# Optimization experiments

Measured on AMD Instinct MI355X. Metric: run time of the kernel, lower is better.

Reference implementation:

```python
import jax, jax.numpy as jnp
import numpy as np

HID, NH, HD = 1024, 16, 64
WIN = 512
DFF, NE, TOPK = 4096, 8, 2
B, S = 1, 2048
EPS = 1e-6


def _rope_rotation_matrix(seq_len, head_dim):
    # Block-diagonal 2x2 rotation matrices per position (standard RoPE as a fused matrix).
    pos = np.arange(seq_len, dtype=np.float64)
    inv_freq = 1.0 / (10000.0 ** (np.arange(0, head_dim, 2, dtype=np.float64) / head_dim))
    ang = pos[:, None] * inv_freq[None, :]            # [S, HD/2]
    c, s = np.cos(ang), np.sin(ang)
    R = np.zeros((seq_len, head_dim, head_dim), np.float32)
    i = np.arange(0, head_dim, 2)
    R[:, i, i] = c
    R[:, i + 1, i + 1] = c
    R[:, i, i + 1] = -s
    R[:, i + 1, i] = s
    return jnp.asarray(R)


def setup_inputs() -> dict:
    key = jax.random.key(0)
    ks = jax.random.split(key, 10)
    init = lambda k, shape, scale=0.02: (jax.random.normal(k, shape, jnp.float32) * scale)
    return {
        "x": jax.random.normal(ks[0], (B, S, HID), jnp.float32),
        "rotation_matrix": _rope_rotation_matrix(S, HD),
        "rms1_w": jnp.ones((HID,), jnp.float32),
        "wq": init(ks[1], (HID, HID)),
        "wk": init(ks[2], (HID, HID)),
        "wv": init(ks[3], (HID, HID)),
        "wo": init(ks[4], (HID, HID)),
        "rms2_w": jnp.ones((HID,), jnp.float32),
        "gate_w": init(ks[5], (HID, NE)),
        "w1": init(ks[6], (NE, HID, DFF)),
        "w2": init(ks[7], (NE, DFF, HID)),
        "w3": init(ks[8], (NE, HID, DFF)),
    }


def _rmsnorm(x, w):
    return x * jax.lax.rsqrt(jnp.mean(x * x, axis=-1, keepdims=True) + EPS) * w


def reference(x, rotation_matrix, rms1_w, wq, wk, wv, wo, rms2_w, gate_w, w1, w2, w3):
    b, s, _ = x.shape
    # --- sliding-window attention with fused RoPE rotation matrix ---
    y = _rmsnorm(x, rms1_w)
    q = (y @ wq).reshape(b, s, NH, HD).transpose(0, 2, 1, 3)  # bhsd
    k = (y @ wk).reshape(b, s, NH, HD).transpose(0, 2, 1, 3)
    v = (y @ wv).reshape(b, s, NH, HD).transpose(0, 2, 1, 3)
    q = jnp.einsum('bhsd,sde->bhse', q, rotation_matrix)
    k = jnp.einsum('bhsd,sde->bhse', k, rotation_matrix)
    scores = jnp.einsum('bhqd,bhkd->bhqk', q, k) / np.float32(np.sqrt(HD))
    idx = jnp.arange(s)
    mask = (idx[:, None] >= idx[None, :]) & (idx[:, None] - idx[None, :] < WIN)
    scores = jnp.where(mask[None, None], scores, jnp.float32(-1e9))
    att = jax.nn.softmax(scores, axis=-1)
    attn_out = jnp.einsum('bhqk,bhkd->bhqd', att, v)
    attn_out = attn_out.transpose(0, 2, 1, 3).reshape(b, s, HID) @ wo
    x = x + attn_out
    # --- MoE SwiGLU FFN with top-k routing ---
    y = _rmsnorm(x, rms2_w)
    t = y.reshape(b * s, HID)                                  # [T, D]
    logits = t @ gate_w                                        # [T, E]
    top_v, top_i = jax.lax.top_k(logits, TOPK)
    gates = jax.nn.softmax(top_v, axis=-1)                     # [T, K]
    w_full = jnp.zeros((b * s, NE), t.dtype).at[
        jnp.arange(b * s)[:, None], top_i].set(gates)          # [T, E] sparse routing weights
    h = jax.nn.silu(jnp.einsum('td,edf->etf', t, w1)) * jnp.einsum('td,edf->etf', t, w3)
    expert_out = jnp.einsum('etf,efd->etd', h, w2)             # [E, T, D]
    moe = jnp.einsum('te,etd->td', w_full, expert_out).reshape(b, s, HID)
    return x + moe
```

## Files before the change

kernel.cpp:

```cpp
#include <hip/hip_runtime.h>
#include <hip/hip_bf16.h>
#include <stdint.h>


#define S_ 2048
#define HID_ 1024
#define NH_ 16
#define HD_ 64
#define WIN_ 512
#define DFF_ 4096
#define NE_ 8

typedef unsigned short u16;
typedef __attribute__((ext_vector_type(8))) short short8;
typedef __attribute__((ext_vector_type(4))) float f32x4;

__device__ __forceinline__ u16 f2bf(float f) {
  union { float f; unsigned u; } v; v.f = f;
  unsigned r = (v.u + 0x7FFFu + ((v.u >> 16) & 1u)) >> 16;
  return (u16)r;
}
__device__ __forceinline__ float bf2f(u16 b) {
  union { unsigned u; float f; } v; v.u = ((unsigned)b) << 16;
  return v.f;
}

__device__ __forceinline__ void gload16(const void* g, void* l) {
  __builtin_amdgcn_global_load_lds(
      (const __attribute__((address_space(1))) void*)g,
      (__attribute__((address_space(3))) void*)l, 16, 0, 0);
}

__global__ __launch_bounds__(256) void convT_f32_k(const float* __restrict__ W,
                                                   u16* __restrict__ WT,
                                                   int K, int N, size_t matStride) {
  __shared__ u16 t[64][66];
  const float* Wm = W + (size_t)blockIdx.z * matStride;
  u16* WTm = WT + (size_t)blockIdx.z * matStride;
  int n0 = blockIdx.x * 64, k0 = blockIdx.y * 64;
  int tid = threadIdx.x;
  int c2 = (tid & 31) * 2, rr = tid >> 5;
#pragma unroll
  for (int it = 0; it < 8; ++it) {
    int r = it * 8 + rr;
    float2 ab = *(const float2*)&Wm[(size_t)(k0 + r) * N + n0 + c2];
    t[c2][r] = f2bf(ab.x);
    t[c2 + 1][r] = f2bf(ab.y);
  }
  __syncthreads();
#pragma unroll
  for (int it = 0; it < 8; ++it) {
    int n = it * 8 + rr;
    unsigned pk = (unsigned)t[n][c2] | ((unsigned)t[n][c2 + 1] << 16);
    *(unsigned*)&WTm[(size_t)(n0 + n) * K + k0 + c2] = pk;
  }
}

__global__ __launch_bounds__(256) void convT_u16_k(const u16* __restrict__ W,
                                                   u16* __restrict__ WT,
                                                   int K, int N, size_t matStride) {
  __shared__ u16 t[64][66];
  const u16* Wm = W + (size_t)blockIdx.z * matStride;
  u16* WTm = WT + (size_t)blockIdx.z * matStride;
  int n0 = blockIdx.x * 64, k0 = blockIdx.y * 64;
  int tid = threadIdx.x;
  int c2 = (tid & 31) * 2, rr = tid >> 5;
#pragma unroll
  for (int it = 0; it < 8; ++it) {
    int r = it * 8 + rr;
    unsigned vv = *(const unsigned*)&Wm[(size_t)(k0 + r) * N + n0 + c2];
    t[c2][r] = (u16)vv;
    t[c2 + 1][r] = (u16)(vv >> 16);
  }
  __syncthreads();
#pragma unroll
  for (int it = 0; it < 8; ++it) {
    int n = it * 8 + rr;
    unsigned pk = (unsigned)t[n][c2] | ((unsigned)t[n][c2 + 1] << 16);
    *(unsigned*)&WTm[(size_t)(n0 + n) * K + k0 + c2] = pk;
  }
}

__global__ __launch_bounds__(256) void rope_tab_k(const float* __restrict__ rot,
                                                  float* __restrict__ cost,
                                                  float* __restrict__ sint) {
  int id = blockIdx.x * 256 + threadIdx.x;
  if (id >= S_ * 32) return;
  int s = id >> 5, j = id & 31;
  cost[id] = rot[(size_t)s * 4096 + (size_t)(2 * j) * 64 + 2 * j];
  sint[id] = rot[(size_t)s * 4096 + (size_t)(2 * j + 1) * 64 + 2 * j];
}

__global__ __launch_bounds__(256) void rms1_k(const float* __restrict__ x,
                                              const float* __restrict__ rw,
                                              u16* __restrict__ y) {
  int row = blockIdx.x, tid = threadIdx.x;
  const float4 v = *(const float4*)&x[(size_t)row * HID_ + tid * 4];
  float ss = v.x * v.x + v.y * v.y + v.z * v.z + v.w * v.w;
#pragma unroll
  for (int o = 32; o; o >>= 1) ss += __shfl_xor(ss, o);
  __shared__ float red[4];
  if ((tid & 63) == 0) red[tid >> 6] = ss;
  __syncthreads();
  float rstd = rsqrtf((red[0] + red[1] + red[2] + red[3]) * (1.f / HID_) + 1e-6f);
  const float4 w4 = *(const float4*)&rw[tid * 4];
  ushort4 o4;
  o4.x = f2bf(v.x * rstd * w4.x);
  o4.y = f2bf(v.y * rstd * w4.y);
  o4.z = f2bf(v.z * rstd * w4.z);
  o4.w = f2bf(v.w * rstd * w4.w);
  *(ushort4*)&y[(size_t)row * HID_ + tid * 4] = o4;
}

__global__ __launch_bounds__(256) void rms2_gate_k(const float* __restrict__ x2,
                                                   const float* __restrict__ rw,
                                                   const float* __restrict__ gw,
                                                   u16* __restrict__ y2,
                                                   float* __restrict__ logits) {
  int row = blockIdx.x, tid = threadIdx.x;
  int wv = tid >> 6, ln = tid & 63;
  const float4 v = *(const float4*)&x2[(size_t)row * HID_ + tid * 4];
  float ss = v.x * v.x + v.y * v.y + v.z * v.z + v.w * v.w;
#pragma unroll
  for (int o = 32; o; o >>= 1) ss += __shfl_xor(ss, o);
  __shared__ float red[4];
  __shared__ float lred[4][8];
  if (ln == 0) red[wv] = ss;
  __syncthreads();
  float rstd = rsqrtf((red[0] + red[1] + red[2] + red[3]) * (1.f / HID_) + 1e-6f);
  const float4 w4 = *(const float4*)&rw[tid * 4];
  float yv[4];
  yv[0] = v.x * rstd * w4.x; yv[1] = v.y * rstd * w4.y;
  yv[2] = v.z * rstd * w4.z; yv[3] = v.w * rstd * w4.w;
  ushort4 o4;
  o4.x = f2bf(yv[0]); o4.y = f2bf(yv[1]); o4.z = f2bf(yv[2]); o4.w = f2bf(yv[3]);
  *(ushort4*)&y2[(size_t)row * HID_ + tid * 4] = o4;
  float le[8] = {0, 0, 0, 0, 0, 0, 0, 0};
  int d0 = tid * 4;
#pragma unroll
  for (int j = 0; j < 4; ++j) {
    const float* grow = &gw[(size_t)(d0 + j) * NE_];
#pragma unroll
    for (int e = 0; e < 8; ++e) le[e] += yv[j] * grow[e];
  }
#pragma unroll
  for (int e = 0; e < 8; ++e) {
    float t = le[e];
#pragma unroll
    for (int o = 32; o; o >>= 1) t += __shfl_xor(t, o);
    le[e] = t;
  }
  if (ln == 0)
#pragma unroll
    for (int e = 0; e < 8; ++e) lred[wv][e] = le[e];
  __syncthreads();
  if (tid < 8)
    logits[(size_t)row * NE_ + tid] =
        lred[0][tid] + lred[1][tid] + lred[2][tid] + lred[3][tid];
}

__global__ __launch_bounds__(256) void topk_k(const float* __restrict__ logits,
                                              int* __restrict__ topi,
                                              float* __restrict__ topg,
                                              int* __restrict__ counts) {
  int t = blockIdx.x * 256 + threadIdx.x;
  if (t >= S_) return;
  const float* lg = &logits[(size_t)t * NE_];
  float v0 = -1e30f; int i0 = 0;
#pragma unroll
  for (int e = 0; e < 8; ++e) {
    float x = lg[e];
    if (x > v0) { v0 = x; i0 = e; }
  }
  float v1 = -1e30f; int i1 = 0;
#pragma unroll
  for (int e = 0; e < 8; ++e) {
    if (e == i0) continue;
    float x = lg[e];
    if (x > v1) { v1 = x; i1 = e; }
  }
  float e1 = __expf(v1 - v0);
  topi[t * 2] = i0; topi[t * 2 + 1] = i1;
  topg[t * 2] = 1.f / (1.f + e1);
  topg[t * 2 + 1] = e1 / (1.f + e1);
  atomicAdd(&counts[i0], 1);
  atomicAdd(&counts[i1], 1);
}

__global__ void prefix_k(const int* __restrict__ counts, int* __restrict__ ebase) {
  if (threadIdx.x == 0) {
    int s = 0;
    for (int e = 0; e < 8; ++e) { ebase[e] = s; s += counts[e]; }
  }
}

__global__ __launch_bounds__(256) void scatter_k(const int* __restrict__ topi,
                                                 const int* __restrict__ ebase,
                                                 int* __restrict__ rank,
                                                 int* __restrict__ slot_token,
                                                 int* __restrict__ slot_of) {
  int t = blockIdx.x * 256 + threadIdx.x;
  if (t >= S_) return;
  for (int k = 0; k < 2; ++k) {
    int e = topi[t * 2 + k];
    int pos = ebase[e] + atomicAdd(&rank[e], 1);
    slot_token[pos] = t;
    slot_of[t * 2 + k] = pos;
  }
}

template <int TPB, int MODE>
__global__ __launch_bounds__(TPB, 2) void gemm5_k(
    const u16* __restrict__ A, const u16* __restrict__ B0,
    const u16* __restrict__ B1, const u16* __restrict__ B2, int K,
    const int* __restrict__ ecnt, const int* __restrict__ ebase,
    const int* __restrict__ slot_token, const float* __restrict__ cost,
    const float* __restrict__ sint, const float* __restrict__ xres,
    float* __restrict__ outf, u16* __restrict__ o0, u16* __restrict__ o1,
    u16* __restrict__ o2) {
  constexpr int NW = TPB / 64;
  constexpr int WN = NW / 2;
  constexpr int BM = TPB / 2;
  constexpr int MROW = BM / 2;
  constexpr int MI = MROW / 16;
  constexpr int MH = MI / 2;
  constexpr int ABYTES = BM * 128;
  __shared__ alignas(16) char smem[ABYTES * 4];
  char* ldsA = smem;
  char* ldsB = smem + 2 * ABYTES;

  int n0 = blockIdx.x * BM, m0 = blockIdx.y * BM;
  int cnt = 0, base = 0;
  const u16* Bp;
  u16* outb = o0;
  int rope = 0;
  if constexpr (MODE == 0) {
    int z = blockIdx.z;
    Bp = (z == 0) ? B0 : (z == 1) ? B1 : B2;
    outb = (z == 0) ? o0 : (z == 1) ? o1 : o2;
    rope = (z < 2) ? 1 : 0;
  } else if constexpr (MODE == 1) {
    Bp = B0;
  } else if constexpr (MODE == 2) {
    int e = blockIdx.z >> 1, mat = blockIdx.z & 1;
    cnt = ecnt[e]; base = ebase[e];
    if (m0 >= cnt) return;
    Bp = (mat ? B1 : B0) + (size_t)e * DFF_ * HID_;
    outb = mat ? o1 : o0;
  } else {
    int e = blockIdx.z;
    cnt = ecnt[e]; base = ebase[e];
    if (m0 >= cnt) return;
    Bp = B0 + (size_t)e * HID_ * DFF_;
  }

  int tid = threadIdx.x, w = tid >> 6, l = tid & 63, lo = l & 15, g = l >> 4;
  int wm = w / WN, wn = w % WN;
  int KT = K >> 6;
  size_t rb = (size_t)K * 2;

  int lrow = l >> 3, lu = l & 7;
  const char* pA[4];
  const char* pB[4];
  int ldOff[4];
#pragma unroll
  for (int j = 0; j < 4; ++j) {
    int rA = j * (BM / 4) + w * 8 + lrow;
    int swz = (lu ^ (rA & 7)) << 4;
    size_t arow;
    if constexpr (MODE == 2) {
      arow = (size_t)slot_token[base + min(m0 + rA, cnt - 1)];
    } else if constexpr (MODE == 3) {
      arow = (size_t)(base + min(m0 + rA, cnt - 1));
    } else {
      arow = (size_t)(m0 + rA);
    }
    pA[j] = (const char*)A + arow * rb + swz;
    pB[j] = (const char*)Bp + (size_t)(n0 + rA) * rb + swz;
    ldOff[j] = (j * (BM / 4) + w * 8) * 128;
  }

  auto stA = [&](int t, int j) {
    gload16(pA[j] + (size_t)t * 128, ldsA + (t & 1) * ABYTES + ldOff[j]);
  };
  auto stB = [&](int t, int j) {
    gload16(pB[j] + (size_t)t * 128, ldsB + (t & 1) * ABYTES + ldOff[j]);
  };
  auto rdA = [&](int d, int mi, int kh) {
    int row = wm * MROW + mi * 16 + lo;
    return *(const short8*)(ldsA + d * ABYTES + row * 128 +
                            (((kh * 4 + g) ^ (row & 7)) << 4));
  };
  auto rdB = [&](int d, int ni, int kh) {
    int row = wn * 64 + ni * 16 + lo;
    return *(const short8*)(ldsB + d * ABYTES + row * 128 +
                            (((kh * 4 + g) ^ (row & 7)) << 4));
  };

  f32x4 acc[MI][4];
#pragma unroll
  for (int i = 0; i < MI; ++i)
#pragma unroll
    for (int j = 0; j < 4; ++j) acc[i][j] = (f32x4){0.f, 0.f, 0.f, 0.f};

  stB(0, 0); stB(0, 1); stB(0, 2); stB(0, 3);
  stA(0, 0); stA(0, 2);
  stA(0, 1); stA(0, 3);
  {
    int t1 = min(1, KT - 1);
    stA(t1, 0); stA(t1, 2);
  }
  asm volatile("s_waitcnt vmcnt(4)" ::: "memory");
  __builtin_amdgcn_s_barrier();

  for (int t = 0; t < KT; ++t) {
    int d = t & 1;
    int tn = min(t + 1, KT - 1);
    int tn2 = min(t + 2, KT - 1);
    short8 afr[MH], bfr[4];
    stB(tn, 0); stB(tn, 1);
#pragma unroll
    for (int i = 0; i < MH; ++i) afr[i] = rdA(d, i, 0);
#pragma unroll
    for (int n = 0; n < 4; ++n) bfr[n] = rdB(d, n, 0);
    asm volatile("s_waitcnt lgkmcnt(0)" ::: "memory");
    __builtin_amdgcn_s_setprio(1);
#pragma unroll
    for (int i = 0; i < MH; ++i)
#pragma unroll
      for (int n = 0; n < 4; ++n)
        acc[i][n] = __builtin_amdgcn_mfma_f32_16x16x32_bf16(afr[i], bfr[n], acc[i][n], 0, 0, 0);
    __builtin_amdgcn_s_setprio(0);
    asm volatile("s_waitcnt vmcnt(4)" ::: "memory");
    __builtin_amdgcn_s_barrier();
    stB(tn, 2); stB(tn, 3);
#pragma unroll
    for (int i = 0; i < MH; ++i) afr[i] = rdA(d, MH + i, 0);
    asm volatile("s_waitcnt lgkmcnt(0)" ::: "memory");
    __builtin_amdgcn_s_setprio(1);
#pragma unroll
    for (int i = 0; i < MH; ++i)
#pragma unroll
      for (int n = 0; n < 4; ++n)
        acc[MH + i][n] = __builtin_amdgcn_mfma_f32_16x16x32_bf16(afr[i], bfr[n], acc[MH + i][n], 0, 0, 0);
    __builtin_amdgcn_s_setprio(0);
    __builtin_amdgcn_s_barrier();
    stA(tn, 1); stA(tn, 3);
#pragma unroll
    for (int i = 0; i < MH; ++i) afr[i] = rdA(d, i, 1);
#pragma unroll
    for (int n = 0; n < 4; ++n) bfr[n] = rdB(d, n, 1);
    asm volatile("s_waitcnt lgkmcnt(0)" ::: "memory");
    __builtin_amdgcn_s_setprio(1);
#pragma unroll
    for (int i = 0; i < MH; ++i)
#pragma unroll
      for (int n = 0; n < 4; ++n)
        acc[i][n] = __builtin_amdgcn_mfma_f32_16x16x32_bf16(afr[i], bfr[n], acc[i][n], 0, 0, 0);
    __builtin_amdgcn_s_setprio(0);
    __builtin_amdgcn_s_barrier();
    stA(tn2, 0); stA(tn2, 2);
#pragma unroll
    for (int i = 0; i < MH; ++i) afr[i] = rdA(d, MH + i, 1);
    asm volatile("s_waitcnt lgkmcnt(0)" ::: "memory");
    __builtin_amdgcn_s_setprio(1);
#pragma unroll
    for (int i = 0; i < MH; ++i)
#pragma unroll
      for (int n = 0; n < 4; ++n)
        acc[MH + i][n] = __builtin_amdgcn_mfma_f32_16x16x32_bf16(afr[i], bfr[n], acc[MH + i][n], 0, 0, 0);
    __builtin_amdgcn_s_setprio(0);
    asm volatile("s_waitcnt vmcnt(4)" ::: "memory");
    __builtin_amdgcn_s_barrier();
  }
  asm volatile("s_waitcnt vmcnt(0) lgkmcnt(0)" ::: "memory");

#pragma unroll
  for (int mi = 0; mi < MI; ++mi) {
    int lr = wm * MROW + mi * 16 + g * 4;
#pragma unroll
    for (int ni = 0; ni < 4; ++ni) {
      int c = n0 + wn * 64 + ni * 16 + lo;
#pragma unroll
      for (int r = 0; r < 4; ++r) {
        float v = acc[mi][ni][r];
        if constexpr (MODE == 0) {
          int row = m0 + lr + r;
          float p = __shfl_xor(v, 1);
          if (rope) {
            int dd = c & 63;
            float co = cost[(size_t)row * 32 + (dd >> 1)];
            float si = sint[(size_t)row * 32 + (dd >> 1)];
            v = (dd & 1) ? (co * v - si * p) : (co * v + si * p);
          }
          outb[((size_t)(c >> 6) * S_ + row) * HD_ + (c & 63)] = f2bf(v);
        } else if constexpr (MODE == 1) {
          int row = m0 + lr + r;
          outf[(size_t)row * HID_ + c] = v + xres[(size_t)row * HID_ + c];
        } else if constexpr (MODE == 2) {
          int m = m0 + lr + r;
          if (m < cnt) outb[(size_t)(base + m) * DFF_ + c] = f2bf(v);
        } else {
          int m = m0 + lr + r;
          if (m < cnt) outb[(size_t)(base + m) * HID_ + c] = f2bf(v);
        }
      }
    }
  }
}

__global__ __launch_bounds__(256) void swiglu_k(u16* __restrict__ h1,
                                                const u16* __restrict__ h3) {
  size_t i = ((size_t)blockIdx.x * 256 + threadIdx.x) * 8;
  short8 a = *(const short8*)(h1 + i);
  short8 b = *(const short8*)(h3 + i);
  short8 o;
#pragma unroll
  for (int j = 0; j < 8; ++j) {
    float x = bf2f((u16)a[j]), y = bf2f((u16)b[j]);
    float s = x / (1.f + __expf(-x));
    o[j] = (short)f2bf(s * y);
  }
  *(short8*)(h1 + i) = o;
}

__global__ __launch_bounds__(256) void attn_k(const u16* __restrict__ qh,
                                              const u16* __restrict__ kh,
                                              const u16* __restrict__ vht,
                                              u16* __restrict__ attn) {
  int qt = blockIdx.x, h = blockIdx.y;
  int tid = threadIdx.x, w = tid >> 6, l = tid & 63, lo = l & 15, g = l >> 4;
  __shared__ alignas(16) char Ks[8192];
  __shared__ alignas(16) char Vs[8192];
  __shared__ alignas(16) char Ps[8192];
  char* Pw = Ps + w * 2048;
  int q0 = qt * 64, qw = q0 + w * 16;
  const u16* qhh = qh + ((size_t)h * S_ + qw) * HD_;
  short8 bq0 = *(const short8*)(qhh + lo * 64 + g * 8);
  short8 bq1 = *(const short8*)(qhh + lo * 64 + 32 + g * 8);
  int q = qw + lo;
  float m_run = -1e30f, l_run = 0.f;
  f32x4 o[4];
#pragma unroll
  for (int i = 0; i < 4; ++i) o[i] = (f32x4){0.f, 0.f, 0.f, 0.f};
  int kt0 = max(0, q0 - (WIN_ - 1)) >> 6;
  for (int kt = kt0; kt <= qt; ++kt) {
    int kb = kt * 64;
    {
      int r0 = w * 16 + (l >> 3), r1 = r0 + 8;
      int uu = l & 7;
      short8 k0v = *(const short8*)(kh + ((size_t)h * S_ + kb + r0) * HD_ + uu * 8);
      short8 k1v = *(const short8*)(kh + ((size_t)h * S_ + kb + r1) * HD_ + uu * 8);
      short8 v0v = *(const short8*)(vht + ((size_t)h * HD_ + r0) * S_ + kb + uu * 8);
      short8 v1v = *(const short8*)(vht + ((size_t)h * HD_ + r1) * S_ + kb + uu * 8);
      *(short8*)(Ks + r0 * 128 + ((uu ^ (r0 & 7)) << 4)) = k0v;
      *(short8*)(Ks + r1 * 128 + ((uu ^ (r1 & 7)) << 4)) = k1v;
      *(short8*)(Vs + r0 * 128 + ((uu ^ (r0 & 7)) << 4)) = v0v;
      *(short8*)(Vs + r1 * 128 + ((uu ^ (r1 & 7)) << 4)) = v1v;
    }
    __syncthreads();
    f32x4 st[4];
#pragma unroll
    for (int kf = 0; kf < 4; ++kf) {
      int key = kf * 16 + lo;
      short8 a0 = *(const short8*)(Ks + key * 128 + ((g ^ (key & 7)) << 4));
      short8 a1 = *(const short8*)(Ks + key * 128 + (((4 + g) ^ (key & 7)) << 4));
      f32x4 z = (f32x4){0.f, 0.f, 0.f, 0.f};
      z = __builtin_amdgcn_mfma_f32_16x16x32_bf16(a0, bq0, z, 0, 0, 0);
      z = __builtin_amdgcn_mfma_f32_16x16x32_bf16(a1, bq1, z, 0, 0, 0);
      st[kf] = z;
    }
    float p[16];
    float tmax = -1e30f;
#pragma unroll
    for (int kf = 0; kf < 4; ++kf)
#pragma unroll
      for (int r = 0; r < 4; ++r) {
        int key = kb + kf * 16 + g * 4 + r;
        float s = st[kf][r] * 0.125f;
        bool okm = (key <= q) && (q - key < WIN_);
        s = okm ? s : -1e30f;
        p[kf * 4 + r] = s;
        tmax = fmaxf(tmax, s);
      }
    tmax = fmaxf(tmax, __shfl_xor(tmax, 16));
    tmax = fmaxf(tmax, __shfl_xor(tmax, 32));
    float m_new = fmaxf(m_run, tmax);
    float corr = __expf(m_run - m_new);
    float tsum = 0.f;
#pragma unroll
    for (int i = 0; i < 16; ++i) {
      float pe = (p[i] > -1e29f) ? __expf(p[i] - m_new) : 0.f;
      p[i] = pe;
      tsum += pe;
    }
    tsum += __shfl_xor(tsum, 16);
    tsum += __shfl_xor(tsum, 32);
    l_run = l_run * corr + tsum;
    m_run = m_new;
#pragma unroll
    for (int kf = 0; kf < 4; ++kf)
#pragma unroll
      for (int pr = 0; pr < 2; ++pr) {
        int keyloc = kf * 16 + g * 4 + pr * 2;
        unsigned pk = (unsigned)f2bf(p[kf * 4 + pr * 2]) |
                      ((unsigned)f2bf(p[kf * 4 + pr * 2 + 1]) << 16);
        *(unsigned*)(Pw + lo * 128 + (((keyloc >> 3) ^ (lo & 7)) << 4) +
                     (keyloc & 7) * 2) = pk;
      }
    float c0 = __shfl(corr, g * 4 + 0), c1 = __shfl(corr, g * 4 + 1);
    float c2 = __shfl(corr, g * 4 + 2), c3 = __shfl(corr, g * 4 + 3);
#pragma unroll
    for (int nf = 0; nf < 4; ++nf) {
      o[nf][0] *= c0; o[nf][1] *= c1; o[nf][2] *= c2; o[nf][3] *= c3;
    }
    short8 ap0 = *(const short8*)(Pw + lo * 128 + ((g ^ (lo & 7)) << 4));
    short8 ap1 = *(const short8*)(Pw + lo * 128 + (((4 + g) ^ (lo & 7)) << 4));
#pragma unroll
    for (int nf = 0; nf < 4; ++nf) {
      int d = nf * 16 + lo;
      short8 v0 = *(const short8*)(Vs + d * 128 + ((g ^ (d & 7)) << 4));
      short8 v1 = *(const short8*)(Vs + d * 128 + (((4 + g) ^ (d & 7)) << 4));
      o[nf] = __builtin_amdgcn_mfma_f32_16x16x32_bf16(ap0, v0, o[nf], 0, 0, 0);
      o[nf] = __builtin_amdgcn_mfma_f32_16x16x32_bf16(ap1, v1, o[nf], 0, 0, 0);
    }
    __syncthreads();
  }
  float linv = 1.f / l_run;
  float i0 = __shfl(linv, g * 4 + 0), i1 = __shfl(linv, g * 4 + 1);
  float i2 = __shfl(linv, g * 4 + 2), i3 = __shfl(linv, g * 4 + 3);
#pragma unroll
  for (int nf = 0; nf < 4; ++nf) {
    int d = nf * 16 + lo;
    attn[(size_t)(qw + g * 4 + 0) * HID_ + h * HD_ + d] = f2bf(o[nf][0] * i0);
    attn[(size_t)(qw + g * 4 + 1) * HID_ + h * HD_ + d] = f2bf(o[nf][1] * i1);
    attn[(size_t)(qw + g * 4 + 2) * HID_ + h * HD_ + d] = f2bf(o[nf][2] * i2);
    attn[(size_t)(qw + g * 4 + 3) * HID_ + h * HD_ + d] = f2bf(o[nf][3] * i3);
  }
}

__global__ __launch_bounds__(256) void combine_k(float* __restrict__ out,
                                                 const u16* __restrict__ eo,
                                                 const int* __restrict__ slot_of,
                                                 const float* __restrict__ topg) {
  int row = blockIdx.x, tid = threadIdx.x;
  int d0 = tid * 4;
  int p0 = slot_of[row * 2], p1 = slot_of[row * 2 + 1];
  float g0 = topg[row * 2], g1 = topg[row * 2 + 1];
  float4 cur = *(float4*)&out[(size_t)row * HID_ + d0];
  ushort4 ea = *(const ushort4*)&eo[(size_t)p0 * HID_ + d0];
  ushort4 eb = *(const ushort4*)&eo[(size_t)p1 * HID_ + d0];
  cur.x += g0 * bf2f(ea.x) + g1 * bf2f(eb.x);
  cur.y += g0 * bf2f(ea.y) + g1 * bf2f(eb.y);
  cur.z += g0 * bf2f(ea.z) + g1 * bf2f(eb.z);
  cur.w += g0 * bf2f(ea.w) + g1 * bf2f(eb.w);
  *(float4*)&out[(size_t)row * HID_ + d0] = cur;
}

extern "C" void kernel_launch(void* const* d_in, const int* in_sizes, int n_in,
                              void* d_out, int out_size, void* d_ws,
                              size_t ws_size, hipStream_t stream) {
  const float* x = (const float*)d_in[0];
  const float* rot = (const float*)d_in[1];
  const float* r1w = (const float*)d_in[2];
  const float* wq = (const float*)d_in[3];
  const float* wk = (const float*)d_in[4];
  const float* wv = (const float*)d_in[5];
  const float* wo = (const float*)d_in[6];
  const float* r2w = (const float*)d_in[7];
  const float* gw = (const float*)d_in[8];
  const float* w1 = (const float*)d_in[9];
  const float* w2 = (const float*)d_in[10];
  const float* w3 = (const float*)d_in[11];
  float* out = (float*)d_out;

  char* ws = (char*)d_ws;
  size_t off = 0;
  auto alloc = [&](size_t bytes) {
    char* p = ws + off;
    off += (bytes + 255) & ~(size_t)255;
    return p;
  };
  const size_t MB4 = (size_t)S_ * HID_ * 2;
  u16* wqT = (u16*)alloc((size_t)HID_ * HID_ * 2);
  u16* wkT = (u16*)alloc((size_t)HID_ * HID_ * 2);
  u16* wvT = (u16*)alloc((size_t)HID_ * HID_ * 2);
  u16* woT = (u16*)alloc((size_t)HID_ * HID_ * 2);
  u16* w1T = (u16*)alloc((size_t)NE_ * DFF_ * HID_ * 2);
  u16* w3T = (u16*)alloc((size_t)NE_ * DFF_ * HID_ * 2);
  u16* w2T = (u16*)alloc((size_t)NE_ * HID_ * DFF_ * 2);
  char* uni = alloc((size_t)2 * S_ * DFF_ * 2);
  u16* ybf = (u16*)(uni);
  u16* qh = (u16*)(uni + MB4);
  u16* kh = (u16*)(uni + 2 * MB4);
  u16* vh = (u16*)(uni + 3 * MB4);
  u16* vht = (u16*)(uni + 4 * MB4);
  u16* attnb = (u16*)(uni + 5 * MB4);
  u16* h3 = (u16*)uni;
  u16* y2bf = (u16*)alloc(MB4);
  u16* h1 = (u16*)alloc((size_t)2 * S_ * DFF_ * 2);
  u16* eo = (u16*)alloc((size_t)2 * S_ * HID_ * 2);
  float* cost = (float*)alloc((size_t)S_ * 32 * 4);
  float* sint = (float*)alloc((size_t)S_ * 32 * 4);
  float* logits = (float*)alloc((size_t)S_ * NE_ * 4);
  int* topi = (int*)alloc((size_t)S_ * 2 * 4);
  float* topg = (float*)alloc((size_t)S_ * 2 * 4);
  int* ints = (int*)alloc(256);
  int* counts = ints;
  int* rank = ints + 8;
  int* ebase = ints + 16;
  int* slot_token = (int*)alloc((size_t)2 * S_ * 4);
  int* slot_of = (int*)alloc((size_t)S_ * 2 * 4);
  (void)ws_size; (void)in_sizes; (void)n_in; (void)out_size;

  hipMemsetAsync(counts, 0, 64, stream);

  convT_f32_k<<<dim3(16, 16, 1), 256, 0, stream>>>(wq, wqT, HID_, HID_, (size_t)HID_ * HID_);
  convT_f32_k<<<dim3(16, 16, 1), 256, 0, stream>>>(wk, wkT, HID_, HID_, (size_t)HID_ * HID_);
  convT_f32_k<<<dim3(16, 16, 1), 256, 0, stream>>>(wv, wvT, HID_, HID_, (size_t)HID_ * HID_);
  convT_f32_k<<<dim3(16, 16, 1), 256, 0, stream>>>(wo, woT, HID_, HID_, (size_t)HID_ * HID_);
  convT_f32_k<<<dim3(64, 16, 8), 256, 0, stream>>>(w1, w1T, HID_, DFF_, (size_t)HID_ * DFF_);
  convT_f32_k<<<dim3(64, 16, 8), 256, 0, stream>>>(w3, w3T, HID_, DFF_, (size_t)HID_ * DFF_);
  convT_f32_k<<<dim3(16, 64, 8), 256, 0, stream>>>(w2, w2T, DFF_, HID_, (size_t)DFF_ * HID_);

  rope_tab_k<<<dim3(256), 256, 0, stream>>>(rot, cost, sint);
  rms1_k<<<dim3(S_), 256, 0, stream>>>(x, r1w, ybf);

  gemm5_k<256, 0><<<dim3(8, 16, 3), 256, 0, stream>>>(
      ybf, wqT, wkT, wvT, HID_, nullptr, nullptr, nullptr, cost, sint, nullptr,
      nullptr, qh, kh, vh);
  convT_u16_k<<<dim3(1, 32, 16), 256, 0, stream>>>(vh, vht, S_, HD_, (size_t)S_ * HD_);

  attn_k<<<dim3(32, 16), 256, 0, stream>>>(qh, kh, vht, attnb);

  gemm5_k<256, 1><<<dim3(8, 16, 1), 256, 0, stream>>>(
      attnb, woT, nullptr, nullptr, HID_, nullptr, nullptr, nullptr, nullptr,
      nullptr, x, out, nullptr, nullptr, nullptr);

  rms2_gate_k<<<dim3(S_), 256, 0, stream>>>(out, r2w, gw, y2bf, logits);
  topk_k<<<dim3(8), 256, 0, stream>>>(logits, topi, topg, counts);
  prefix_k<<<dim3(1), 64, 0, stream>>>(counts, ebase);
  scatter_k<<<dim3(8), 256, 0, stream>>>(topi, ebase, rank, slot_token, slot_of);

  gemm5_k<512, 2><<<dim3(16, 8, 16), 512, 0, stream>>>(
      y2bf, w1T, w3T, nullptr, HID_, counts, ebase, slot_token, nullptr,
      nullptr, nullptr, nullptr, h1, h3, nullptr);
  swiglu_k<<<dim3(8192), 256, 0, stream>>>(h1, h3);
  gemm5_k<256, 3><<<dim3(8, 16, 8), 256, 0, stream>>>(
      h1, w2T, nullptr, nullptr, DFF_, counts, ebase, slot_token, nullptr,
      nullptr, nullptr, nullptr, eo, nullptr, nullptr);
  combine_k<<<dim3(S_), 256, 0, stream>>>(out, eo, slot_of, topg);
}
```

Measured before the change: 454.6 us.

## Add triple-buffered K32 GEMM, fuse routing kernels, batch QKVO weight conversion

Adds a new 128x128-tile GEMM kernel with a three-stage LDS ring and K=32 steps. It replaces the old GEMM for the QKV, output-projection and expert-down GEMMs, aiming for better latency hiding and occupancy of 3 blocks per CU. The topk, prefix and scatter launches are merged into one single-block routing kernel that uses shared-memory atomics, which also removes a memset. The four attention weight transposes are batched into one launch, and the transpose kernels now use float4 vectorized loads. The trade-off is a serial single-block routing step and a new GEMM schedule that has not been tuned.

```diff
diff --git a/kernel.cpp b/kernel.cpp
--- a/kernel.cpp
+++ b/kernel.cpp
@@ -34,25 +34,57 @@
 __global__ __launch_bounds__(256) void convT_f32_k(const float* __restrict__ W,
                                                    u16* __restrict__ WT,
                                                    int K, int N, size_t matStride) {
-  __shared__ u16 t[64][66];
+  __shared__ u16 t[64][72];
   const float* Wm = W + (size_t)blockIdx.z * matStride;
   u16* WTm = WT + (size_t)blockIdx.z * matStride;
   int n0 = blockIdx.x * 64, k0 = blockIdx.y * 64;
   int tid = threadIdx.x;
-  int c2 = (tid & 31) * 2, rr = tid >> 5;
-#pragma unroll
-  for (int it = 0; it < 8; ++it) {
-    int r = it * 8 + rr;
-    float2 ab = *(const float2*)&Wm[(size_t)(k0 + r) * N + n0 + c2];
-    t[c2][r] = f2bf(ab.x);
-    t[c2 + 1][r] = f2bf(ab.y);
-  }
-  __syncthreads();
-#pragma unroll
-  for (int it = 0; it < 8; ++it) {
-    int n = it * 8 + rr;
-    unsigned pk = (unsigned)t[n][c2] | ((unsigned)t[n][c2 + 1] << 16);
-    *(unsigned*)&WTm[(size_t)(n0 + n) * K + k0 + c2] = pk;
+  int cw = (tid & 15) * 4, rr = tid >> 4;
+#pragma unroll
+  for (int p = 0; p < 4; ++p) {
+    int r = p * 16 + rr;
+    float4 v = *(const float4*)&Wm[(size_t)(k0 + r) * N + n0 + cw];
+    t[cw][r] = f2bf(v.x);
+    t[cw + 1][r] = f2bf(v.y);
+    t[cw + 2][r] = f2bf(v.z);
+    t[cw + 3][r] = f2bf(v.w);
+  }
+  __syncthreads();
+#pragma unroll
+  for (int p = 0; p < 4; ++p) {
+    int n = p * 16 + rr;
+    ushort4 pk = *(const ushort4*)&t[n][cw];
+    *(ushort4*)&WTm[(size_t)(n0 + n) * K + k0 + cw] = pk;
+  }
+}
+
+__global__ __launch_bounds__(256) void convT_qkvo_k(const float* __restrict__ wq,
+                                                    const float* __restrict__ wk,
+                                                    const float* __restrict__ wv,
+                                                    const float* __restrict__ wo,
+                                                    u16* __restrict__ outT) {
+  __shared__ u16 t[64][72];
+  int z = blockIdx.z;
+  const float* Wm = (z == 0) ? wq : (z == 1) ? wk : (z == 2) ? wv : wo;
+  u16* WTm = outT + (size_t)z * HID_ * HID_;
+  int n0 = blockIdx.x * 64, k0 = blockIdx.y * 64;
+  int tid = threadIdx.x;
+  int cw = (tid & 15) * 4, rr = tid >> 4;
+#pragma unroll
+  for (int p = 0; p < 4; ++p) {
+    int r = p * 16 + rr;
+    float4 v = *(const float4*)&Wm[(size_t)(k0 + r) * HID_ + n0 + cw];
+    t[cw][r] = f2bf(v.x);
+    t[cw + 1][r] = f2bf(v.y);
+    t[cw + 2][r] = f2bf(v.z);
+    t[cw + 3][r] = f2bf(v.w);
+  }
+  __syncthreads();
+#pragma unroll
+  for (int p = 0; p < 4; ++p) {
+    int n = p * 16 + rr;
+    ushort4 pk = *(const ushort4*)&t[n][cw];
+    *(ushort4*)&WTm[(size_t)(n0 + n) * HID_ + k0 + cw] = pk;
   }
 }
 
@@ -159,77 +191,73 @@
         lred[0][tid] + lred[1][tid] + lred[2][tid] + lred[3][tid];
 }
 
-__global__ __launch_bounds__(256) void topk_k(const float* __restrict__ logits,
-                                              int* __restrict__ topi,
-                                              float* __restrict__ topg,
-                                              int* __restrict__ counts) {
-  int t = blockIdx.x * 256 + threadIdx.x;
-  if (t >= S_) return;
-  const float* lg = &logits[(size_t)t * NE_];
-  float v0 = -1e30f; int i0 = 0;
-#pragma unroll
-  for (int e = 0; e < 8; ++e) {
-    float x = lg[e];
-    if (x > v0) { v0 = x; i0 = e; }
-  }
-  float v1 = -1e30f; int i1 = 0;
-#pragma unroll
-  for (int e = 0; e < 8; ++e) {
-    if (e == i0) continue;
-    float x = lg[e];
-    if (x > v1) { v1 = x; i1 = e; }
-  }
-  float e1 = __expf(v1 - v0);
-  topi[t * 2] = i0; topi[t * 2 + 1] = i1;
-  topg[t * 2] = 1.f / (1.f + e1);
-  topg[t * 2 + 1] = e1 / (1.f + e1);
-  atomicAdd(&counts[i0], 1);
-  atomicAdd(&counts[i1], 1);
-}
-
-__global__ void prefix_k(const int* __restrict__ counts, int* __restrict__ ebase) {
-  if (threadIdx.x == 0) {
+__global__ __launch_bounds__(1024) void route_k(const float* __restrict__ logits,
+                                                int* __restrict__ topi,
+                                                float* __restrict__ topg,
+                                                int* __restrict__ counts,
+                                                int* __restrict__ ebase,
+                                                int* __restrict__ slot_token,
+                                                int* __restrict__ slot_of) {
+  __shared__ int cnt[8], bas[8], rnk[8];
+  int tid = threadIdx.x;
+  if (tid < 8) { cnt[tid] = 0; rnk[tid] = 0; }
+  __syncthreads();
+  int e0[2], e1[2];
+  float g0[2], g1[2];
+#pragma unroll
+  for (int s = 0; s < 2; ++s) {
+    int t = tid * 2 + s;
+    const float* lg = &logits[(size_t)t * NE_];
+    float v0 = -1e30f; int i0 = 0;
+#pragma unroll
+    for (int e = 0; e < 8; ++e) {
+      float x = lg[e];
+      if (x > v0) { v0 = x; i0 = e; }
+    }
+    float v1 = -1e30f; int i1 = 0;
+#pragma unroll
+    for (int e = 0; e < 8; ++e) {
+      if (e == i0) continue;
+      float x = lg[e];
+      if (x > v1) { v1 = x; i1 = e; }
+    }
+    float ex = __expf(v1 - v0);
+    e0[s] = i0; e1[s] = i1;
+    g0[s] = 1.f / (1.f + ex);
+    g1[s] = ex / (1.f + ex);
+    topi[t * 2] = i0; topi[t * 2 + 1] = i1;
+    topg[t * 2] = g0[s]; topg[t * 2 + 1] = g1[s];
+    atomicAdd(&cnt[i0], 1);
+    atomicAdd(&cnt[i1], 1);
+  }
+  __syncthreads();
+  if (tid == 0) {
     int s = 0;
-    for (int e = 0; e < 8; ++e) { ebase[e] = s; s += counts[e]; }
-  }
-}
-
-__global__ __launch_bounds__(256) void scatter_k(const int* __restrict__ topi,
-                                                 const int* __restrict__ ebase,
-                                                 int* __restrict__ rank,
-                                                 int* __restrict__ slot_token,
-                                                 int* __restrict__ slot_of) {
-  int t = blockIdx.x * 256 + threadIdx.x;
-  if (t >= S_) return;
-  for (int k = 0; k < 2; ++k) {
-    int e = topi[t * 2 + k];
-    int pos = ebase[e] + atomicAdd(&rank[e], 1);
-    slot_token[pos] = t;
-    slot_of[t * 2 + k] = pos;
-  }
-}
-
-template <int TPB, int MODE>
-__global__ __launch_bounds__(TPB, 2) void gemm5_k(
+    for (int e = 0; e < 8; ++e) { bas[e] = s; s += cnt[e]; }
+  }
+  __syncthreads();
+#pragma unroll
+  for (int s = 0; s < 2; ++s) {
+    int t = tid * 2 + s;
+    int p0 = bas[e0[s]] + atomicAdd(&rnk[e0[s]], 1);
+    int p1 = bas[e1[s]] + atomicAdd(&rnk[e1[s]], 1);
+    slot_token[p0] = t; slot_token[p1] = t;
+    slot_of[t * 2] = p0; slot_of[t * 2 + 1] = p1;
+  }
+  if (tid < 8) { counts[tid] = cnt[tid]; ebase[tid] = bas[tid]; }
+}
+
+template <int MODE>
+__global__ __launch_bounds__(256, 3) void gemm3_k(
     const u16* __restrict__ A, const u16* __restrict__ B0,
     const u16* __restrict__ B1, const u16* __restrict__ B2, int K,
     const int* __restrict__ ecnt, const int* __restrict__ ebase,
-    const int* __restrict__ slot_token, const float* __restrict__ cost,
-    const float* __restrict__ sint, const float* __restrict__ xres,
-    float* __restrict__ outf, u16* __restrict__ o0, u16* __restrict__ o1,
-    u16* __restrict__ o2) {
-  constexpr int NW = TPB / 64;
-  constexpr int WN = NW / 2;
-  constexpr int BM = TPB / 2;
-  constexpr int MROW = BM / 2;
-  constexpr int MI = MROW / 16;
-  constexpr int MH = MI / 2;
-  constexpr int ABYTES = BM * 128;
-  __shared__ alignas(16) char smem[ABYTES * 4];
-  char* ldsA = smem;
-  char* ldsB = smem + 2 * ABYTES;
-
-  int n0 = blockIdx.x * BM, m0 = blockIdx.y * BM;
+    const float* __restrict__ cost, const float* __restrict__ sint,
+    const float* __restrict__ xres, float* __restrict__ outf,
+    u16* __restrict__ o0, u16* __restrict__ o1, u16* __restrict__ o2) {
+  __shared__ alignas(16) char smem[49152];
+
+  int n0 = blockIdx.x * 128, m0 = blockIdx.y * 128;
   int cnt = 0, base = 0;
   const u16* Bp;
   u16* outb = o0;
@@ -241,17 +269,145 @@
     rope = (z < 2) ? 1 : 0;
   } else if constexpr (MODE == 1) {
     Bp = B0;
-  } else if constexpr (MODE == 2) {
+  } else {
+    int e = blockIdx.z;
+    cnt = ecnt[e]; base = ebase[e];
+    if (m0 >= cnt) return;
+    Bp = B0 + (size_t)e * HID_ * DFF_;
+  }
+
+  int tid = threadIdx.x, w = tid >> 6, l = tid & 63, lo = l & 15, g = l >> 4;
+  int wm = w >> 1, wn = w & 1;
+  int KT = K >> 5;
+  size_t rb = (size_t)K * 2;
+
+  int lrow = l >> 2, lu = l & 3;
+  const char* pA[2];
+  const char* pB[2];
+  int ldOff[2];
+#pragma unroll
+  for (int j = 0; j < 2; ++j) {
+    int rA = j * 64 + w * 16 + lrow;
+    int swz = (lu ^ ((rA >> 1) & 3)) << 4;
+    size_t arow;
+    if constexpr (MODE == 3) {
+      arow = (size_t)(base + min(m0 + rA, cnt - 1));
+    } else {
+      arow = (size_t)(m0 + rA);
+    }
+    pA[j] = (const char*)A + arow * rb + swz;
+    pB[j] = (const char*)Bp + (size_t)(n0 + rA) * rb + swz;
+    ldOff[j] = (j * 64 + w * 16) * 64;
+  }
+
+  auto stage = [&](int t) {
+    char* s = smem + (t % 3) * 16384;
+    size_t kb = (size_t)t * 64;
+    gload16(pA[0] + kb, s + ldOff[0]);
+    gload16(pA[1] + kb, s + ldOff[1]);
+    gload16(pB[0] + kb, s + 8192 + ldOff[0]);
+    gload16(pB[1] + kb, s + 8192 + ldOff[1]);
+  };
+
+  f32x4 acc[4][4];
+#pragma unroll
+  for (int i = 0; i < 4; ++i)
+#pragma unroll
+    for (int j = 0; j < 4; ++j) acc[i][j] = (f32x4){0.f, 0.f, 0.f, 0.f};
+
+  stage(0);
+  stage(min(1, KT - 1));
+  asm volatile("s_waitcnt vmcnt(4)" ::: "memory");
+  __builtin_amdgcn_s_barrier();
+
+  for (int t = 0; t < KT; ++t) {
+    char* s = smem + (t % 3) * 16384;
+    stage(min(t + 2, KT - 1));
+    short8 afr[4], bfr[4];
+#pragma unroll
+    for (int mi = 0; mi < 4; ++mi) {
+      int r = wm * 64 + mi * 16 + lo;
+      afr[mi] = *(const short8*)(s + r * 64 + ((g ^ ((r >> 1) & 3)) << 4));
+    }
+#pragma unroll
+    for (int ni = 0; ni < 4; ++ni) {
+      int r = wn * 64 + ni * 16 + lo;
+      bfr[ni] = *(const short8*)(s + 8192 + r * 64 + ((g ^ ((r >> 1) & 3)) << 4));
+    }
+    asm volatile("s_waitcnt lgkmcnt(0)" ::: "memory");
+    __builtin_amdgcn_s_setprio(1);
+#pragma unroll
+    for (int mi = 0; mi < 4; ++mi)
+#pragma unroll
+      for (int ni = 0; ni < 4; ++ni)
+        acc[mi][ni] = __builtin_amdgcn_mfma_f32_16x16x32_bf16(afr[mi], bfr[ni], acc[mi][ni], 0, 0, 0);
+    __builtin_amdgcn_s_setprio(0);
+    if (t + 1 < KT)
+      asm volatile("s_waitcnt vmcnt(4)" ::: "memory");
+    else
+      asm volatile("s_waitcnt vmcnt(0)" ::: "memory");
+    __builtin_amdgcn_s_barrier();
+  }
+  asm volatile("s_waitcnt vmcnt(0) lgkmcnt(0)" ::: "memory");
+
+#pragma unroll
+  for (int mi = 0; mi < 4; ++mi) {
+    int lr = wm * 64 + mi * 16 + g * 4;
+#pragma unroll
+    for (int ni = 0; ni < 4; ++ni) {
+      int c = n0 + wn * 64 + ni * 16 + lo;
+#pragma unroll
+      for (int r = 0; r < 4; ++r) {
+        float v = acc[mi][ni][r];
+        if constexpr (MODE == 0) {
+          int row = m0 + lr + r;
+          float p = __shfl_xor(v, 1);
+          if (rope) {
+            int dd = c & 63;
+            float co = cost[(size_t)row * 32 + (dd >> 1)];
+            float si = sint[(size_t)row * 32 + (dd >> 1)];
+            v = (dd & 1) ? (co * v - si * p) : (co * v + si * p);
+          }
+          outb[((size_t)(c >> 6) * S_ + row) * HD_ + (c & 63)] = f2bf(v);
+        } else if constexpr (MODE == 1) {
+          int row = m0 + lr + r;
+          outf[(size_t)row * HID_ + c] = v + xres[(size_t)row * HID_ + c];
+        } else {
+          int m = m0 + lr + r;
+          if (m < cnt) outb[(size_t)(base + m) * HID_ + c] = f2bf(v);
+        }
+      }
+    }
+  }
+}
+
+template <int TPB, int MODE>
+__global__ __launch_bounds__(TPB, 2) void gemm5_k(
+    const u16* __restrict__ A, const u16* __restrict__ B0,
+    const u16* __restrict__ B1, int K, const int* __restrict__ ecnt,
+    const int* __restrict__ ebase, const int* __restrict__ slot_token,
+    u16* __restrict__ o0, u16* __restrict__ o1) {
+  constexpr int NW = TPB / 64;
+  constexpr int WN = NW / 2;
+  constexpr int BM = TPB / 2;
+  constexpr int MROW = BM / 2;
+  constexpr int MI = MROW / 16;
+  constexpr int MH = MI / 2;
+  constexpr int ABYTES = BM * 128;
+  __shared__ alignas(16) char smem[ABYTES * 4];
+  char* ldsA = smem;
+  char* ldsB = smem + 2 * ABYTES;
+
+  int n0 = blockIdx.x * BM, m0 = blockIdx.y * BM;
+  int cnt = 0, base = 0;
+  const u16* Bp;
+  u16* outb;
+  {
     int e = blockIdx.z >> 1, mat = blockIdx.z & 1;
     cnt = ecnt[e]; base = ebase[e];
     if (m0 >= cnt) return;
     Bp = (mat ? B1 : B0) + (size_t)e * DFF_ * HID_;
     outb = mat ? o1 : o0;
-  } else {
-    int e = blockIdx.z;
-    cnt = ecnt[e]; base = ebase[e];
-    if (m0 >= cnt) return;
-    Bp = B0 + (size_t)e * HID_ * DFF_;
   }
 
   int tid = threadIdx.x, w = tid >> 6, l = tid & 63, lo = l & 15, g = l >> 4;
@@ -267,14 +423,7 @@
   for (int j = 0; j < 4; ++j) {
     int rA = j * (BM / 4) + w * 8 + lrow;
     int swz = (lu ^ (rA & 7)) << 4;
-    size_t arow;
-    if constexpr (MODE == 2) {
-      arow = (size_t)slot_token[base + min(m0 + rA, cnt - 1)];
-    } else if constexpr (MODE == 3) {
-      arow = (size_t)(base + min(m0 + rA, cnt - 1));
-    } else {
-      arow = (size_t)(m0 + rA);
-    }
+    size_t arow = (size_t)slot_token[base + min(m0 + rA, cnt - 1)];
     pA[j] = (const char*)A + arow * rb + swz;
     pB[j] = (const char*)Bp + (size_t)(n0 + rA) * rb + swz;
     ldOff[j] = (j * (BM / 4) + w * 8) * 128;
@@ -383,27 +532,8 @@
       int c = n0 + wn * 64 + ni * 16 + lo;
 #pragma unroll
       for (int r = 0; r < 4; ++r) {
-        float v = acc[mi][ni][r];
-        if constexpr (MODE == 0) {
-          int row = m0 + lr + r;
-          float p = __shfl_xor(v, 1);
-          if (rope) {
-            int dd = c & 63;
-            float co = cost[(size_t)row * 32 + (dd >> 1)];
-            float si = sint[(size_t)row * 32 + (dd >> 1)];
-            v = (dd & 1) ? (co * v - si * p) : (co * v + si * p);
-          }
-          outb[((size_t)(c >> 6) * S_ + row) * HD_ + (c & 63)] = f2bf(v);
-        } else if constexpr (MODE == 1) {
-          int row = m0 + lr + r;
-          outf[(size_t)row * HID_ + c] = v + xres[(size_t)row * HID_ + c];
-        } else if constexpr (MODE == 2) {
-          int m = m0 + lr + r;
-          if (m < cnt) outb[(size_t)(base + m) * DFF_ + c] = f2bf(v);
-        } else {
-          int m = m0 + lr + r;
-          if (m < cnt) outb[(size_t)(base + m) * HID_ + c] = f2bf(v);
-        }
+        int m = m0 + lr + r;
+        if (m < cnt) outb[(size_t)(base + m) * DFF_ + c] = f2bf(acc[mi][ni][r]);
       }
     }
   }
@@ -582,10 +712,11 @@
     return p;
   };
   const size_t MB4 = (size_t)S_ * HID_ * 2;
-  u16* wqT = (u16*)alloc((size_t)HID_ * HID_ * 2);
-  u16* wkT = (u16*)alloc((size_t)HID_ * HID_ * 2);
-  u16* wvT = (u16*)alloc((size_t)HID_ * HID_ * 2);
-  u16* woT = (u16*)alloc((size_t)HID_ * HID_ * 2);
+  u16* wqkvoT = (u16*)alloc((size_t)4 * HID_ * HID_ * 2);
+  u16* wqT = wqkvoT;
+  u16* wkT = wqkvoT + (size_t)HID_ * HID_;
+  u16* wvT = wqkvoT + (size_t)2 * HID_ * HID_;
+  u16* woT = wqkvoT + (size_t)3 * HID_ * HID_;
   u16* w1T = (u16*)alloc((size_t)NE_ * DFF_ * HID_ * 2);
   u16* w3T = (u16*)alloc((size_t)NE_ * DFF_ * HID_ * 2);
   u16* w2T = (u16*)alloc((size_t)NE_ * HID_ * DFF_ * 2);
@@ -607,18 +738,12 @@
   float* topg = (float*)alloc((size_t)S_ * 2 * 4);
   int* ints = (int*)alloc(256);
   int* counts = ints;
-  int* rank = ints + 8;
-  int* ebase = ints + 16;
+  int* ebase = ints + 8;
   int* slot_token = (int*)alloc((size_t)2 * S_ * 4);
   int* slot_of = (int*)alloc((size_t)S_ * 2 * 4);
   (void)ws_size; (void)in_sizes; (void)n_in; (void)out_size;
 
-  hipMemsetAsync(counts, 0, 64, stream);
-
-  convT_f32_k<<<dim3(16, 16, 1), 256, 0, stream>>>(wq, wqT, HID_, HID_, (size_t)HID_ * HID_);
-  convT_f32_k<<<dim3(16, 16, 1), 256, 0, stream>>>(wk, wkT, HID_, HID_, (size_t)HID_ * HID_);
-  convT_f32_k<<<dim3(16, 16, 1), 256, 0, stream>>>(wv, wvT, HID_, HID_, (size_t)HID_ * HID_);
-  convT_f32_k<<<dim3(16, 16, 1), 256, 0, stream>>>(wo, woT, HID_, HID_, (size_t)HID_ * HID_);
+  convT_qkvo_k<<<dim3(16, 16, 4), 256, 0, stream>>>(wq, wk, wv, wo, wqkvoT);
   convT_f32_k<<<dim3(64, 16, 8), 256, 0, stream>>>(w1, w1T, HID_, DFF_, (size_t)HID_ * DFF_);
   convT_f32_k<<<dim3(64, 16, 8), 256, 0, stream>>>(w3, w3T, HID_, DFF_, (size_t)HID_ * DFF_);
   convT_f32_k<<<dim3(16, 64, 8), 256, 0, stream>>>(w2, w2T, DFF_, HID_, (size_t)DFF_ * HID_);
@@ -626,28 +751,26 @@
   rope_tab_k<<<dim3(256), 256, 0, stream>>>(rot, cost, sint);
   rms1_k<<<dim3(S_), 256, 0, stream>>>(x, r1w, ybf);
 
-  gemm5_k<256, 0><<<dim3(8, 16, 3), 256, 0, stream>>>(
-      ybf, wqT, wkT, wvT, HID_, nullptr, nullptr, nullptr, cost, sint, nullptr,
+  gemm3_k<0><<<dim3(8, 16, 3), 256, 0, stream>>>(
+      ybf, wqT, wkT, wvT, HID_, nullptr, nullptr, cost, sint, nullptr,
       nullptr, qh, kh, vh);
   convT_u16_k<<<dim3(1, 32, 16), 256, 0, stream>>>(vh, vht, S_, HD_, (size_t)S_ * HD_);
 
   attn_k<<<dim3(32, 16), 256, 0, stream>>>(qh, kh, vht, attnb);
 
-  gemm5_k<256, 1><<<dim3(8, 16, 1), 256, 0, stream>>>(
+  gemm3_k<1><<<dim3(8, 16, 1), 256, 0, stream>>>(
       attnb, woT, nullptr, nullptr, HID_, nullptr, nullptr, nullptr, nullptr,
-      nullptr, x, out, nullptr, nullptr, nullptr);
+      x, out, nullptr, nullptr, nullptr);
 
   rms2_gate_k<<<dim3(S_), 256, 0, stream>>>(out, r2w, gw, y2bf, logits);
-  topk_k<<<dim3(8), 256, 0, stream>>>(logits, topi, topg, counts);
-  prefix_k<<<dim3(1), 64, 0, stream>>>(counts, ebase);
-  scatter_k<<<dim3(8), 256, 0, stream>>>(topi, ebase, rank, slot_token, slot_of);
+  route_k<<<dim3(1), 1024, 0, stream>>>(logits, topi, topg, counts, ebase,
+                                        slot_token, slot_of);
 
   gemm5_k<512, 2><<<dim3(16, 8, 16), 512, 0, stream>>>(
-      y2bf, w1T, w3T, nullptr, HID_, counts, ebase, slot_token, nullptr,
-      nullptr, nullptr, nullptr, h1, h3, nullptr);
+      y2bf, w1T, w3T, HID_, counts, ebase, slot_token, h1, h3);
   swiglu_k<<<dim3(8192), 256, 0, stream>>>(h1, h3);
-  gemm5_k<256, 3><<<dim3(8, 16, 8), 256, 0, stream>>>(
-      h1, w2T, nullptr, nullptr, DFF_, counts, ebase, slot_token, nullptr,
-      nullptr, nullptr, nullptr, eo, nullptr, nullptr);
+  gemm3_k<3><<<dim3(8, 16, 8), 256, 0, stream>>>(
+      h1, w2T, nullptr, nullptr, DFF_, counts, ebase, nullptr, nullptr,
+      nullptr, nullptr, eo, nullptr, nullptr);
   combine_k<<<dim3(S_), 256, 0, stream>>>(out, eo, slot_of, topg);
 }
```

Measured after the change: 458.4 us. About the same (+0.8%).
